# Optimization experiments

Measured on AMD Instinct MI355X. Metric: run time of the kernel, lower is better.

Reference implementation:

```python
import jax, jax.numpy as jnp
import numpy as np
from jax import lax

SEQ, B, IN, H = 2048, 256, 64, 128

def setup_inputs() -> dict:
    key = jax.random.key(0)
    ks = jax.random.split(key, 7)
    seq = jax.random.normal(ks[0], (SEQ, B, IN), dtype=jnp.float32)
    # layer 0: lin_in [H, IN], lin_hidden [H, H] (torch Linear weight layout)
    W_in0 = jax.random.normal(ks[1], (H, IN), dtype=jnp.float32) / np.sqrt(IN)
    W_h0 = jax.random.normal(ks[2], (H, H), dtype=jnp.float32) / np.sqrt(H)
    # layer 1: lin_in [H, H], lin_hidden [H, H]
    W_in1 = jax.random.normal(ks[3], (H, H), dtype=jnp.float32) / np.sqrt(H)
    W_h1 = jax.random.normal(ks[4], (H, H), dtype=jnp.float32) / np.sqrt(H)
    # learned init states, shape [1, H] each (nn.Parameter(torch.zeros(1, H)))
    h0_0 = jnp.zeros((1, H), dtype=jnp.float32)
    h0_1 = jnp.zeros((1, H), dtype=jnp.float32)
    return {"sequence": seq, "W_in0": W_in0, "W_h0": W_h0,
            "W_in1": W_in1, "W_h1": W_h1, "h0_0": h0_0, "h0_1": h0_1}

def _run_layer(x_seq, W_in, W_h, h0):
    # x_seq: [T, B, D_in]; precompute input projection once (same math as per-step)
    xin = jnp.einsum('tbi,hi->tbh', x_seq, W_in)  # [T, B, H]
    h_init = jnp.broadcast_to(h0, (x_seq.shape[1], W_h.shape[0]))
    def step(h, xt):
        h_new = jax.nn.gelu(h @ W_h.T + xt, approximate=False)
        return h_new, h_new
    h_last, ys = lax.scan(step, h_init, xin)
    return ys, h_last

def reference(sequence, W_in0, W_h0, W_in1, W_h1, h0_0, h0_1):
    y0, h0_last = _run_layer(sequence, W_in0, W_h0, h0_0)
    y1, h1_last = _run_layer(y0, W_in1, W_h1, h0_1)
    final_hiddens = jnp.stack([h0_last, h1_last])  # [num_layers, B, H]
    return y1, final_hiddens
```

## Files before the change

### kernel.cpp

```cpp
#include <hip/hip_runtime.h>
#include <math.h>

#define SEQT 2048
#define BATCH 256
#define INDIM 64
#define HDIM 128

typedef float v2f __attribute__((ext_vector_type(2)));

__device__ __forceinline__ float gelu_fast(float x) {
    const float ax = __builtin_fabsf(x);
    const float z  = ax * 0.70710678118654752f;
    const float t  = __builtin_amdgcn_rcpf(__builtin_fmaf(0.3275911f, z, 1.0f));
    float p = __builtin_fmaf(1.061405429f, t, -1.453152027f);
    p = __builtin_fmaf(p, t, 1.421413741f);
    p = __builtin_fmaf(p, t, -0.284496736f);
    p = __builtin_fmaf(p, t, 0.254829592f);
    p = p * t;
    const float e = __builtin_amdgcn_exp2f(z * z * -1.44269504088896f);
    const float erfv = __builtin_fmaf(-p, e, 1.0f);
    return __builtin_fmaf(0.5f * ax, erfv, 0.5f * x);
}

__device__ __forceinline__ v2f gelu2(v2f s) {
    v2f r;
    r.x = gelu_fast(s.x);
    r.y = gelu_fast(s.y);
    return r;
}

__device__ __forceinline__ void pk_lo(v2f& acc, v2f w, v2f hp) {
    asm("v_pk_fma_f32 %0, %1, %2, %0 op_sel:[0,0,0] op_sel_hi:[1,0,1]"
        : "+v"(acc) : "v"(w), "v"(hp));
}
__device__ __forceinline__ void pk_hi(v2f& acc, v2f w, v2f hp) {
    asm("v_pk_fma_f32 %0, %1, %2, %0 op_sel:[0,1,0] op_sel_hi:[1,1,1]"
        : "+v"(acc) : "v"(w), "v"(hp));
}

__device__ __forceinline__ v2f dotu64(const v2f* __restrict__ w2, const float* hsrc) {
    v2f a0 = {0.f, 0.f}, a1 = {0.f, 0.f}, a2 = {0.f, 0.f}, a3 = {0.f, 0.f};
    #pragma unroll
    for (int j = 0; j < 64; j += 4) {
        v2f p0 = *reinterpret_cast<const v2f*>(&hsrc[j]);
        v2f p1 = *reinterpret_cast<const v2f*>(&hsrc[j + 2]);
        pk_lo(a0, w2[j],     p0);
        pk_hi(a1, w2[j + 1], p0);
        pk_lo(a2, w2[j + 2], p1);
        pk_hi(a3, w2[j + 3], p1);
    }
    return (a0 + a1) + (a2 + a3);
}

__global__ __launch_bounds__(448, 1)
__attribute__((amdgpu_waves_per_eu(1, 2)))
void rnn_scan_kernel(
    const float* __restrict__ seq,
    const float* __restrict__ Win0, const float* __restrict__ Wh0,
    const float* __restrict__ Win1, const float* __restrict__ Wh1,
    const float* __restrict__ h00, const float* __restrict__ h01,
    float* __restrict__ out)
{
    const int b = blockIdx.x;
    const int tid = threadIdx.x;
    const int wv = tid >> 6;
    const int l = tid & 63;

    __shared__ __align__(16) v2f red0[2][2][64];
    __shared__ __align__(16) v2f red1[2][2][64];
    __shared__ __align__(16) v2f red2[2][2][64];
    __shared__ __align__(16) v2f x0ring[4][64];
    __shared__ __align__(16) float h0buf[2][HDIM];
    __shared__ __align__(16) float hc[4][HDIM];
    __shared__ __align__(16) float xring[4][INDIM];

    v2f w2[64];
    {
        const float* W;
        int stride, c0;
        if (wv < 2)      { W = Wh0;  stride = HDIM;  c0 = (wv & 1) * 64; }
        else if (wv < 4) { W = Wh1;  stride = HDIM;  c0 = (wv & 1) * 64; }
        else if (wv < 6) { W = Win1; stride = HDIM;  c0 = (wv & 1) * 64; }
        else             { W = Win0; stride = INDIM; c0 = 0; }
        const float* ra = &W[(2 * l) * stride + c0];
        const float* rb = &W[(2 * l + 1) * stride + c0];
        #pragma unroll
        for (int j = 0; j < 64; j += 4) {
            float4 a = *reinterpret_cast<const float4*>(&ra[j]);
            float4 bq = *reinterpret_cast<const float4*>(&rb[j]);
            w2[j]     = (v2f){a.x, bq.x};
            w2[j + 1] = (v2f){a.y, bq.y};
            w2[j + 2] = (v2f){a.z, bq.z};
            w2[j + 3] = (v2f){a.w, bq.w};
        }
    }

    float xC = 0.f;
    if (wv < 2) {
        *reinterpret_cast<v2f*>(&hc[wv][2 * l]) = *reinterpret_cast<const v2f*>(&h00[2 * l]);
    } else if (wv < 4) {
        *reinterpret_cast<v2f*>(&hc[wv][2 * l]) = *reinterpret_cast<const v2f*>(&h01[2 * l]);
    } else if (wv == 6) {
        const size_t base = (size_t)b * INDIM + l;
        xring[0][l] = seq[base];
        xring[1][l] = seq[(size_t)1 * BATCH * INDIM + base];
        xring[2][l] = seq[(size_t)2 * BATCH * INDIM + base];
        xC          = seq[(size_t)3 * BATCH * INDIM + base];
        x0ring[0][l] = dotu64(w2, &xring[0][0]);
    }
    __syncthreads();

    const size_t YSZ = (size_t)SEQT * BATCH * HDIM;

    for (int t = 0; t <= SEQT + 2; ++t) {
        const int par = t & 1;

        if (wv < 2) {
            if (t >= 1 && t <= SEQT) {
                v2f s = red0[par ^ 1][0][l] + red0[par ^ 1][1][l] + x0ring[(t - 1) & 3][l];
                v2f h2 = gelu2(s);
                *reinterpret_cast<v2f*>(&hc[wv][2 * l]) = h2;
                if (wv == 1) *reinterpret_cast<v2f*>(&h0buf[(t - 1) & 1][2 * l]) = h2;
                if (wv == 0 && t == SEQT)
                    *reinterpret_cast<v2f*>(&out[YSZ + (size_t)b * HDIM + 2 * l]) = h2;
            }
            if (t <= SEQT - 1) {
                v2f acc = dotu64(w2, &hc[wv][(wv & 1) * 64]);
                red0[par][wv & 1][l] = acc;
            }
        } else if (wv < 4) {
            if (t >= 3) {
                v2f s = red2[par ^ 1][0][l] + red2[par ^ 1][1][l]
                      + red1[par ^ 1][0][l] + red1[par ^ 1][1][l];
                v2f h2 = gelu2(s);
                *reinterpret_cast<v2f*>(&hc[wv][2 * l]) = h2;
                if (wv == 2) {
                    const int tt = t - 3;
                    *reinterpret_cast<v2f*>(&out[((size_t)tt * BATCH + b) * HDIM + 2 * l]) = h2;
                    if (t == SEQT + 2)
                        *reinterpret_cast<v2f*>(
                            &out[YSZ + (size_t)BATCH * HDIM + (size_t)b * HDIM + 2 * l]) = h2;
                }
            }
            if (t >= 2 && t <= SEQT + 1) {
                v2f acc = dotu64(w2, &hc[wv][(wv & 1) * 64]);
                red2[par][wv & 1][l] = acc;
            }
        } else if (wv < 6) {
            if (t >= 2 && t <= SEQT + 1) {
                const int kh = wv & 1;
                v2f acc = dotu64(w2, &h0buf[(t - 2) & 1][kh * 64]);
                red1[(t - 2) & 1][kh][l] = acc;
            }
        } else {
            if (t <= SEQT - 2) {
                v2f acc = dotu64(w2, &xring[(t + 1) & 3][0]);
                x0ring[(t + 1) & 3][l] = acc;
                if (t + 3 <= SEQT - 1) {
                    xring[(t + 3) & 3][l] = xC;
                    int tn = t + 4; if (tn > SEQT - 1) tn = SEQT - 1;
                    xC = seq[(size_t)tn * BATCH * INDIM + (size_t)b * INDIM + l];
                }
            }
        }
        __syncthreads();
    }
}

extern "C" void kernel_launch(void* const* d_in, const int* in_sizes, int n_in,
                              void* d_out, int out_size, void* d_ws, size_t ws_size,
                              hipStream_t stream) {
    const float* seq  = (const float*)d_in[0];
    const float* Win0 = (const float*)d_in[1];
    const float* Wh0  = (const float*)d_in[2];
    const float* Win1 = (const float*)d_in[3];
    const float* Wh1  = (const float*)d_in[4];
    const float* h00  = (const float*)d_in[5];
    const float* h01  = (const float*)d_in[6];

    rnn_scan_kernel<<<dim3(BATCH), dim3(448), 0, stream>>>(
        seq, Win0, Wh0, Win1, Wh1, h00, h01, (float*)d_out);
}
```

Measured before the change: 1.215 ms.

## Repartition RNN scan to one wave per matrix with full-row dot products

Reduces the block from 7 waves to 4, with each wave holding a full 128-wide weight row pair in registers (256 VGPRs of weights). This removes the cross-wave partial-sum reduction buffers and their extra LDS traffic. The pipeline is reorganized with ring buffers and deeper stage offsets. Each wave now does twice the serial FMA chain per step, which lengthens the critical path per barrier but cuts the number of LDS exchanges and waves per barrier.

Result: slower. 3.103 ms (+155.3%).

```diff
diff --git a/kernel.cpp b/kernel.cpp
--- a/kernel.cpp
+++ b/kernel.cpp
@@ -38,22 +38,37 @@
         : "+v"(acc) : "v"(w), "v"(hp));
 }
 
-__device__ __forceinline__ v2f dotu64(const v2f* __restrict__ w2, const float* hsrc) {
-    v2f a0 = {0.f, 0.f}, a1 = {0.f, 0.f}, a2 = {0.f, 0.f}, a3 = {0.f, 0.f};
+__device__ __forceinline__ v2f dot128(const v2f* __restrict__ w2, const float* hsrc) {
+    v2f a0 = {0.f,0.f}, a1 = {0.f,0.f}, a2 = {0.f,0.f}, a3 = {0.f,0.f};
+    v2f a4 = {0.f,0.f}, a5 = {0.f,0.f}, a6 = {0.f,0.f}, a7 = {0.f,0.f};
+    #pragma unroll
+    for (int j = 0; j < 128; j += 8) {
+        v2f p0 = *reinterpret_cast<const v2f*>(&hsrc[j]);
+        v2f p1 = *reinterpret_cast<const v2f*>(&hsrc[j + 2]);
+        v2f p2 = *reinterpret_cast<const v2f*>(&hsrc[j + 4]);
+        v2f p3 = *reinterpret_cast<const v2f*>(&hsrc[j + 6]);
+        pk_lo(a0, w2[j],     p0);  pk_hi(a1, w2[j + 1], p0);
+        pk_lo(a2, w2[j + 2], p1);  pk_hi(a3, w2[j + 3], p1);
+        pk_lo(a4, w2[j + 4], p2);  pk_hi(a5, w2[j + 5], p2);
+        pk_lo(a6, w2[j + 6], p3);  pk_hi(a7, w2[j + 7], p3);
+    }
+    return ((a0 + a1) + (a2 + a3)) + ((a4 + a5) + (a6 + a7));
+}
+
+__device__ __forceinline__ v2f dot64(const v2f* __restrict__ w2, const float* hsrc) {
+    v2f a0 = {0.f,0.f}, a1 = {0.f,0.f}, a2 = {0.f,0.f}, a3 = {0.f,0.f};
     #pragma unroll
     for (int j = 0; j < 64; j += 4) {
         v2f p0 = *reinterpret_cast<const v2f*>(&hsrc[j]);
         v2f p1 = *reinterpret_cast<const v2f*>(&hsrc[j + 2]);
-        pk_lo(a0, w2[j],     p0);
-        pk_hi(a1, w2[j + 1], p0);
-        pk_lo(a2, w2[j + 2], p1);
-        pk_hi(a3, w2[j + 3], p1);
+        pk_lo(a0, w2[j],     p0);  pk_hi(a1, w2[j + 1], p0);
+        pk_lo(a2, w2[j + 2], p1);  pk_hi(a3, w2[j + 3], p1);
     }
     return (a0 + a1) + (a2 + a3);
 }
 
-__global__ __launch_bounds__(448, 1)
-__attribute__((amdgpu_waves_per_eu(1, 2)))
+__global__ __launch_bounds__(256, 1)
+__attribute__((amdgpu_waves_per_eu(1, 1)))
 void rnn_scan_kernel(
     const float* __restrict__ seq,
     const float* __restrict__ Win0, const float* __restrict__ Wh0,
@@ -66,24 +81,29 @@
     const int wv = tid >> 6;
     const int l = tid & 63;
 
-    __shared__ __align__(16) v2f red0[2][2][64];
-    __shared__ __align__(16) v2f red1[2][2][64];
-    __shared__ __align__(16) v2f red2[2][2][64];
-    __shared__ __align__(16) v2f x0ring[4][64];
-    __shared__ __align__(16) float h0buf[2][HDIM];
-    __shared__ __align__(16) float hc[4][HDIM];
+    __shared__ __align__(16) float h0ring[4][HDIM];
+    __shared__ __align__(16) float h1ring[4][HDIM];
+    __shared__ __align__(16) v2f   p1ring[4][64];
+    __shared__ __align__(16) v2f   x0ring[4][64];
     __shared__ __align__(16) float xring[4][INDIM];
 
-    v2f w2[64];
-    {
-        const float* W;
-        int stride, c0;
-        if (wv < 2)      { W = Wh0;  stride = HDIM;  c0 = (wv & 1) * 64; }
-        else if (wv < 4) { W = Wh1;  stride = HDIM;  c0 = (wv & 1) * 64; }
-        else if (wv < 6) { W = Win1; stride = HDIM;  c0 = (wv & 1) * 64; }
-        else             { W = Win0; stride = INDIM; c0 = 0; }
-        const float* ra = &W[(2 * l) * stride + c0];
-        const float* rb = &W[(2 * l + 1) * stride + c0];
+    v2f w2[128];
+    if (wv < 3) {
+        const float* W = (wv == 0) ? Wh0 : (wv == 1) ? Wh1 : Win1;
+        const float* ra = &W[(2 * l) * HDIM];
+        const float* rb = &W[(2 * l + 1) * HDIM];
+        #pragma unroll
+        for (int j = 0; j < 128; j += 4) {
+            float4 a = *reinterpret_cast<const float4*>(&ra[j]);
+            float4 bq = *reinterpret_cast<const float4*>(&rb[j]);
+            w2[j]     = (v2f){a.x, bq.x};
+            w2[j + 1] = (v2f){a.y, bq.y};
+            w2[j + 2] = (v2f){a.z, bq.z};
+            w2[j + 3] = (v2f){a.w, bq.w};
+        }
+    } else {
+        const float* ra = &Win0[(2 * l) * INDIM];
+        const float* rb = &Win0[(2 * l + 1) * INDIM];
         #pragma unroll
         for (int j = 0; j < 64; j += 4) {
             float4 a = *reinterpret_cast<const float4*>(&ra[j]);
@@ -95,71 +115,56 @@
         }
     }
 
-    float xC = 0.f;
-    if (wv < 2) {
-        *reinterpret_cast<v2f*>(&hc[wv][2 * l]) = *reinterpret_cast<const v2f*>(&h00[2 * l]);
-    } else if (wv < 4) {
-        *reinterpret_cast<v2f*>(&hc[wv][2 * l]) = *reinterpret_cast<const v2f*>(&h01[2 * l]);
-    } else if (wv == 6) {
+    float xA = 0.f, xB = 0.f;
+    if (wv == 0) {
+        *reinterpret_cast<v2f*>(&h0ring[3][2 * l]) = *reinterpret_cast<const v2f*>(&h00[2 * l]);
+    } else if (wv == 1) {
+        *reinterpret_cast<v2f*>(&h1ring[3][2 * l]) = *reinterpret_cast<const v2f*>(&h01[2 * l]);
+    } else if (wv == 3) {
         const size_t base = (size_t)b * INDIM + l;
         xring[0][l] = seq[base];
         xring[1][l] = seq[(size_t)1 * BATCH * INDIM + base];
-        xring[2][l] = seq[(size_t)2 * BATCH * INDIM + base];
-        xC          = seq[(size_t)3 * BATCH * INDIM + base];
-        x0ring[0][l] = dotu64(w2, &xring[0][0]);
+        xA          = seq[(size_t)2 * BATCH * INDIM + base];
+        xB          = seq[(size_t)3 * BATCH * INDIM + base];
     }
     __syncthreads();
 
     const size_t YSZ = (size_t)SEQT * BATCH * HDIM;
 
-    for (int t = 0; t <= SEQT + 2; ++t) {
-        const int par = t & 1;
-
-        if (wv < 2) {
-            if (t >= 1 && t <= SEQT) {
-                v2f s = red0[par ^ 1][0][l] + red0[par ^ 1][1][l] + x0ring[(t - 1) & 3][l];
-                v2f h2 = gelu2(s);
-                *reinterpret_cast<v2f*>(&hc[wv][2 * l]) = h2;
-                if (wv == 1) *reinterpret_cast<v2f*>(&h0buf[(t - 1) & 1][2 * l]) = h2;
-                if (wv == 0 && t == SEQT)
+    for (int t = 0; t <= SEQT + 3; ++t) {
+        if (wv == 0) {
+            const int s = t - 2;
+            if (s >= 0 && s <= SEQT - 1) {
+                v2f acc = dot128(w2, h0ring[(s - 1) & 3]);
+                v2f h2 = gelu2(acc + x0ring[s & 3][l]);
+                *reinterpret_cast<v2f*>(&h0ring[s & 3][2 * l]) = h2;
+                if (s == SEQT - 1)
                     *reinterpret_cast<v2f*>(&out[YSZ + (size_t)b * HDIM + 2 * l]) = h2;
             }
-            if (t <= SEQT - 1) {
-                v2f acc = dotu64(w2, &hc[wv][(wv & 1) * 64]);
-                red0[par][wv & 1][l] = acc;
+        } else if (wv == 1) {
+            const int r = t - 4;
+            if (r >= 0 && r <= SEQT - 1) {
+                v2f acc = dot128(w2, h1ring[(r - 1) & 3]);
+                v2f h2 = gelu2(acc + p1ring[r & 3][l]);
+                *reinterpret_cast<v2f*>(&h1ring[r & 3][2 * l]) = h2;
+                *reinterpret_cast<v2f*>(&out[((size_t)r * BATCH + b) * HDIM + 2 * l]) = h2;
+                if (r == SEQT - 1)
+                    *reinterpret_cast<v2f*>(
+                        &out[YSZ + (size_t)BATCH * HDIM + (size_t)b * HDIM + 2 * l]) = h2;
             }
-        } else if (wv < 4) {
-            if (t >= 3) {
-                v2f s = red2[par ^ 1][0][l] + red2[par ^ 1][1][l]
-                      + red1[par ^ 1][0][l] + red1[par ^ 1][1][l];
-                v2f h2 = gelu2(s);
-                *reinterpret_cast<v2f*>(&hc[wv][2 * l]) = h2;
-                if (wv == 2) {
-                    const int tt = t - 3;
-                    *reinterpret_cast<v2f*>(&out[((size_t)tt * BATCH + b) * HDIM + 2 * l]) = h2;
-                    if (t == SEQT + 2)
-                        *reinterpret_cast<v2f*>(
-                            &out[YSZ + (size_t)BATCH * HDIM + (size_t)b * HDIM + 2 * l]) = h2;
-                }
-            }
-            if (t >= 2 && t <= SEQT + 1) {
-                v2f acc = dotu64(w2, &hc[wv][(wv & 1) * 64]);
-                red2[par][wv & 1][l] = acc;
-            }
-        } else if (wv < 6) {
-            if (t >= 2 && t <= SEQT + 1) {
-                const int kh = wv & 1;
-                v2f acc = dotu64(w2, &h0buf[(t - 2) & 1][kh * 64]);
-                red1[(t - 2) & 1][kh][l] = acc;
+        } else if (wv == 2) {
+            const int u = t - 3;
+            if (u >= 0 && u <= SEQT - 1) {
+                p1ring[u & 3][l] = dot128(w2, h0ring[u & 3]);
             }
         } else {
-            if (t <= SEQT - 2) {
-                v2f acc = dotu64(w2, &xring[(t + 1) & 3][0]);
-                x0ring[(t + 1) & 3][l] = acc;
-                if (t + 3 <= SEQT - 1) {
-                    xring[(t + 3) & 3][l] = xC;
+            if (t <= SEQT - 1) {
+                x0ring[t & 3][l] = dot64(w2, xring[t & 3]);
+                if (t + 2 <= SEQT - 1) {
+                    xring[(t + 2) & 3][l] = xA;
+                    xA = xB;
                     int tn = t + 4; if (tn > SEQT - 1) tn = SEQT - 1;
-                    xC = seq[(size_t)tn * BATCH * INDIM + (size_t)b * INDIM + l];
+                    xB = seq[(size_t)tn * BATCH * INDIM + (size_t)b * INDIM + l];
                 }
             }
         }
@@ -178,6 +183,6 @@
     const float* h00  = (const float*)d_in[5];
     const float* h01  = (const float*)d_in[6];
 
-    rnn_scan_kernel<<<dim3(BATCH), dim3(448), 0, stream>>>(
+    rnn_scan_kernel<<<dim3(BATCH), dim3(256), 0, stream>>>(
         seq, Win0, Wh0, Win1, Wh1, h00, h01, (float*)d_out);
 }
```
